# Kernel optimization log

Hardware: AMD Instinct MI355X
Metric: run time of the kernel (lower is better)

## Reference

```python
import jax, jax.numpy as jnp
import numpy as np

B, S, D, H, O = 2048, 512, 128, 64, 8
EPS = 1e-5


def setup_inputs() -> dict:
    key = jax.random.key(0)
    ks = jax.random.split(key, 8)
    sc = lambda k, shape, s: jax.random.normal(k, shape, jnp.float32) * s
    return {
        "x": jax.random.normal(ks[0], (B, S, D), jnp.float32),
        "h0": jnp.zeros((1, B, H), jnp.float32),
        # nn.RNN params (single layer, relu nonlinearity)
        "W_ih": sc(ks[1], (H, D), 1.0 / np.sqrt(H)),
        "W_hh": sc(ks[2], (H, H), 1.0 / np.sqrt(H)),
        "b_ih": jnp.zeros((H,), jnp.float32),
        "b_hh": jnp.zeros((H,), jnp.float32),
        # fc head: BatchNorm1d(H) -> Linear(H, H//4) -> ReLU
        "bn1_g": jnp.ones((H,), jnp.float32),
        "bn1_b": jnp.zeros((H,), jnp.float32),
        "fc1_W": sc(ks[3], (H // 4, H), 1.0 / np.sqrt(H)),
        "fc1_b": jnp.zeros((H // 4,), jnp.float32),
        # fc2 head: BatchNorm1d(H//4) -> Linear(H//4, O)
        "bn2_g": jnp.ones((H // 4,), jnp.float32),
        "bn2_b": jnp.zeros((H // 4,), jnp.float32),
        "fc2_W": sc(ks[4], (O, H // 4), 1.0 / np.sqrt(H // 4)),
        "fc2_b": jnp.zeros((O,), jnp.float32),
    }


def _batchnorm(x, g, b):
    # BatchNorm1d in training mode: batch statistics over the batch dim.
    mu = x.mean(0)
    var = x.var(0)  # biased variance, matching torch normalization
    return (x - mu) * jax.lax.rsqrt(var + EPS) * g + b


def reference(x, h0, W_ih, W_hh, b_ih, b_hh, bn1_g, bn1_b, fc1_W, fc1_b,
              bn2_g, bn2_b, fc2_W, fc2_b):
    # Precompute the input projection for all timesteps in one big GEMM.
    xp = jnp.einsum('bsd,hd->sbh', x, W_ih) + b_ih + b_hh  # [S, B, H]

    def step(h, xt):
        h = jax.nn.relu(xt + h @ W_hh.T)  # [B, H]
        return h, None

    hT, _ = jax.lax.scan(step, h0[0], xp)  # last hidden == out[:, -1, :]

    z = _batchnorm(hT, bn1_g, bn1_b)
    z = jax.nn.relu(z @ fc1_W.T + fc1_b)
    z = _batchnorm(z, bn2_g, bn2_b)
    out = z @ fc2_W.T + fc2_b  # [B, O]
    return out, hT[None]  # hidden_state shaped [num_layers, B, H]
```

## Files before the change

### kernel.cpp

```cpp
#include <hip/hip_runtime.h>

#define B_ 2048
#define S_ 512
#define D_ 128
#define H_ 64
#define O_ 8
#define EPS 1e-5f

#define CHUNK 16
#define NCHUNK (S_ / CHUNK)
#define PSTRIDE 68

typedef __attribute__((ext_vector_type(8))) short bf16x8;
typedef __attribute__((ext_vector_type(4))) float f32x4;

__device__ __forceinline__ unsigned pk_bf16(float a, float b) {
  unsigned ua = __builtin_bit_cast(unsigned, a) + 0x8000u;
  unsigned ub = __builtin_bit_cast(unsigned, b) + 0x8000u;
  return (ua >> 16) | (ub & 0xffff0000u);
}

__device__ __forceinline__ bf16x8 pack8(f32x4 a, f32x4 b) {
  union { bf16x8 v; unsigned u[4]; } t;
  t.u[0] = pk_bf16(a[0], a[1]);
  t.u[1] = pk_bf16(a[2], a[3]);
  t.u[2] = pk_bf16(b[0], b[1]);
  t.u[3] = pk_bf16(b[2], b[3]);
  return t.v;
}

__global__ __launch_bounds__(512, 2) void rnn_fused(
    const float* __restrict__ x, const float* __restrict__ h0,
    const float* __restrict__ W_ih, const float* __restrict__ W_hh,
    const float* __restrict__ b_ih, const float* __restrict__ b_hh,
    float* __restrict__ hT) {
  extern __shared__ float Plds[];
  const int tid = threadIdx.x;
  const int w = tid >> 6;
  const int lane = tid & 63;
  const int q = lane >> 4;
  const int c = lane & 15;
  const int row = blockIdx.x * 16 + c;

  const float* xrow = x + (size_t)row * (S_ * D_) + q * 8;
  bf16x8 Aih[4][4];
  f32x4 bias[4];
  bf16x8 Ahh[4][2];
  bf16x8 Bh[2];
  f32x4 acc[4];

  if (w < 7) {
#pragma unroll
    for (int jt = 0; jt < 4; ++jt)
#pragma unroll
      for (int kt = 0; kt < 4; ++kt) {
        const float* p = W_ih + (jt * 16 + c) * D_ + kt * 32 + q * 8;
        Aih[jt][kt] = pack8(*(const f32x4*)p, *(const f32x4*)(p + 4));
      }
#pragma unroll
    for (int jt = 0; jt < 4; ++jt) {
      f32x4 bi = *(const f32x4*)(b_ih + jt * 16 + q * 4);
      f32x4 bh = *(const f32x4*)(b_hh + jt * 16 + q * 4);
      bias[jt] = bi + bh;
    }
  } else {
#pragma unroll
    for (int jt = 0; jt < 4; ++jt)
#pragma unroll
      for (int kt = 0; kt < 2; ++kt) {
        const float* p = W_hh + (jt * 16 + c) * H_ + kt * 32 + q * 4;
        Ahh[jt][kt] = pack8(*(const f32x4*)p, *(const f32x4*)(p + 16));
      }
    const float* h0r = h0 + (size_t)row * H_;
#pragma unroll
    for (int kt = 0; kt < 2; ++kt)
      Bh[kt] = pack8(*(const f32x4*)(h0r + kt * 32 + q * 4),
                     *(const f32x4*)(h0r + kt * 32 + 16 + q * 4));
  }

  f32x4 xb[2][8];
  auto loadx = [&](f32x4* d, int t) {
    const float* p = xrow + (size_t)t * D_;
#pragma unroll
    for (int kt = 0; kt < 4; ++kt) {
      d[2 * kt]     = *(const f32x4*)(p + kt * 32);
      d[2 * kt + 1] = *(const f32x4*)(p + kt * 32 + 4);
    }
  };

  auto pstep = [&](const f32x4* xd, int s, int buf) {
    bf16x8 Bx[4];
#pragma unroll
    for (int kt = 0; kt < 4; ++kt) Bx[kt] = pack8(xd[2 * kt], xd[2 * kt + 1]);
    f32x4 a[4];
#pragma unroll
    for (int jt = 0; jt < 4; ++jt) a[jt] = bias[jt];
#pragma unroll
    for (int kt = 0; kt < 4; ++kt)
#pragma unroll
      for (int jt = 0; jt < 4; ++jt)
        a[jt] = __builtin_amdgcn_mfma_f32_16x16x32_bf16(Aih[jt][kt], Bx[kt], a[jt], 0, 0, 0);
    float* dst = Plds + ((size_t)(buf * CHUNK + s) * 16 + c) * PSTRIDE + q * 4;
#pragma unroll
    for (int jt = 0; jt < 4; ++jt)
      *(f32x4*)(dst + jt * 16) = a[jt];
  };

  const int ns = (CHUNK - 1 - w) / 7 + 1;
  auto produce = [&](int ck, int buf) {
    const int t0 = ck * CHUNK;
    loadx(xb[0], t0 + w);
#pragma unroll
    for (int i = 0; i < 3; ++i) {
      if (i < ns) {
        if (i + 1 < ns) loadx(xb[(i + 1) & 1], t0 + w + 7 * (i + 1));
        pstep(xb[i & 1], w + 7 * i, buf);
      }
    }
  };

  auto consume = [&](int buf) {
    const float* Pb = Plds + (size_t)buf * CHUNK * 16 * PSTRIDE + c * PSTRIDE + q * 4;
    f32x4 accP[4];
#pragma unroll
    for (int jt = 0; jt < 4; ++jt) accP[jt] = *(const f32x4*)(Pb + jt * 16);
#pragma unroll 1
    for (int s = 0; s < CHUNK; ++s) {
      f32x4 accN[4];
#pragma unroll
      for (int jt = 0; jt < 4; ++jt) accN[jt] = accP[jt];
      if (s + 1 < CHUNK) {
        const float* Pn = Pb + (size_t)(s + 1) * 16 * PSTRIDE;
#pragma unroll
        for (int jt = 0; jt < 4; ++jt) accN[jt] = *(const f32x4*)(Pn + jt * 16);
      }
#pragma unroll
      for (int jt = 0; jt < 4; ++jt)
        acc[jt] = __builtin_amdgcn_mfma_f32_16x16x32_bf16(Ahh[jt][0], Bh[0], accP[jt], 0, 0, 0);
#pragma unroll
      for (int jt = 0; jt < 4; ++jt)
        acc[jt] = __builtin_amdgcn_mfma_f32_16x16x32_bf16(Ahh[jt][1], Bh[1], acc[jt], 0, 0, 0);
#pragma unroll
      for (int jt = 0; jt < 4; ++jt)
#pragma unroll
        for (int e = 0; e < 4; ++e)
          acc[jt][e] = __builtin_fmaxf(acc[jt][e], 0.0f);
      Bh[0] = pack8(acc[0], acc[1]);
      Bh[1] = pack8(acc[2], acc[3]);
#pragma unroll
      for (int jt = 0; jt < 4; ++jt) accP[jt] = accN[jt];
    }
  };

  if (w < 7) produce(0, 0);
  __syncthreads();
  for (int ck = 0; ck < NCHUNK; ++ck) {
    if (w < 7) {
      if (ck + 1 < NCHUNK) produce(ck + 1, (ck + 1) & 1);
    } else {
      consume(ck & 1);
    }
    __syncthreads();
  }

  if (w == 7) {
    float* op = hT + (size_t)row * H_;
#pragma unroll
    for (int jt = 0; jt < 4; ++jt)
      *(f32x4*)(op + jt * 16 + q * 4) = acc[jt];
  }
}

__global__ void bn1_stats(const float* __restrict__ hT, float* __restrict__ ws) {
  __shared__ float ls[4][64], ls2[4][64];
  int tid = threadIdx.x;
  int j = tid & 63, rg = tid >> 6;
  int b0 = blockIdx.x * 128;
  float s = 0.f, s2 = 0.f;
  for (int i = 0; i < 32; ++i) {
    float v = hT[(size_t)(b0 + rg + i * 4) * H_ + j];
    s += v; s2 += v * v;
  }
  ls[rg][j] = s; ls2[rg][j] = s2;
  __syncthreads();
  if (tid < 64) {
    float a = ls[0][tid] + ls[1][tid] + ls[2][tid] + ls[3][tid];
    float a2 = ls2[0][tid] + ls2[1][tid] + ls2[2][tid] + ls2[3][tid];
    atomicAdd(&ws[tid], a);
    atomicAdd(&ws[64 + tid], a2);
  }
}

__global__ void fc1_bn2(const float* __restrict__ hT, const float* __restrict__ bn1_g,
                        const float* __restrict__ bn1_b, const float* __restrict__ fc1_W,
                        const float* __restrict__ fc1_b, float* __restrict__ ws) {
  __shared__ float sh[1024], sw[1024], sc[64], sf[64], zz[256];
  int tid = threadIdx.x;
  int base = blockIdx.x * 1024;
  for (int i = tid; i < 1024; i += 256) { sh[i] = hT[base + i]; sw[i] = fc1_W[i]; }
  if (tid < 64) {
    float m = ws[tid] * (1.f / B_);
    float v = ws[64 + tid] * (1.f / B_) - m * m;
    float scl = bn1_g[tid] * rsqrtf(v + EPS);
    sc[tid] = scl;
    sf[tid] = bn1_b[tid] - m * scl;
  }
  __syncthreads();
  int r = tid >> 4, f = tid & 15;
  float a = fc1_b[f];
#pragma unroll 16
  for (int j = 0; j < 64; ++j)
    a += (sh[r * 64 + j] * sc[j] + sf[j]) * sw[f * 64 + j];
  a = fmaxf(a, 0.f);
  ws[160 + blockIdx.x * 256 + tid] = a;
  zz[tid] = a;
  __syncthreads();
  if (tid < 16) {
    float s = 0.f, s2 = 0.f;
    for (int rr = 0; rr < 16; ++rr) { float v = zz[rr * 16 + tid]; s += v; s2 += v * v; }
    atomicAdd(&ws[128 + tid], s);
    atomicAdd(&ws[144 + tid], s2);
  }
}

__global__ void fc2_out(const float* __restrict__ ws, const float* __restrict__ bn2_g,
                        const float* __restrict__ bn2_b, const float* __restrict__ fc2_W,
                        const float* __restrict__ fc2_b, float* __restrict__ out) {
  __shared__ float sc2[16], sf2[16], w2[128], b2[8];
  int tid = threadIdx.x;
  if (tid < 16) {
    float m = ws[128 + tid] * (1.f / B_);
    float v = ws[144 + tid] * (1.f / B_) - m * m;
    float scl = bn2_g[tid] * rsqrtf(v + EPS);
    sc2[tid] = scl;
    sf2[tid] = bn2_b[tid] - m * scl;
  }
  if (tid < 128) w2[tid] = fc2_W[tid];
  if (tid < 8) b2[tid] = fc2_b[tid];
  __syncthreads();
  int gid = blockIdx.x * 256 + tid;
  int r = gid >> 3, o = gid & 7;
  const float* z = ws + 160 + r * 16;
  float a = b2[o];
#pragma unroll
  for (int f = 0; f < 16; ++f)
    a += (z[f] * sc2[f] + sf2[f]) * w2[o * 16 + f];
  out[gid] = a;
}

extern "C" void kernel_launch(void* const* d_in, const int* in_sizes, int n_in,
                              void* d_out, int out_size, void* d_ws, size_t ws_size,
                              hipStream_t stream) {
  (void)in_sizes; (void)n_in; (void)out_size; (void)ws_size;
  const float* x     = (const float*)d_in[0];
  const float* h0    = (const float*)d_in[1];
  const float* W_ih  = (const float*)d_in[2];
  const float* W_hh  = (const float*)d_in[3];
  const float* b_ih  = (const float*)d_in[4];
  const float* b_hh  = (const float*)d_in[5];
  const float* bn1_g = (const float*)d_in[6];
  const float* bn1_b = (const float*)d_in[7];
  const float* fc1_W = (const float*)d_in[8];
  const float* fc1_b = (const float*)d_in[9];
  const float* bn2_g = (const float*)d_in[10];
  const float* bn2_b = (const float*)d_in[11];
  const float* fc2_W = (const float*)d_in[12];
  const float* fc2_b = (const float*)d_in[13];

  float* out = (float*)d_out;
  float* hT  = out + B_ * O_;
  float* ws  = (float*)d_ws;

  const int pbytes = 2 * CHUNK * 16 * PSTRIDE * 4;
  static bool attr_done = false;
  hipFuncSetAttribute((const void*)rnn_fused,
                      hipFuncAttributeMaxDynamicSharedMemorySize, pbytes);
  (void)attr_done;

  hipMemsetAsync(d_ws, 0, 160 * sizeof(float), stream);
  rnn_fused<<<B_ / 16, 512, pbytes, stream>>>(x, h0, W_ih, W_hh, b_ih, b_hh, hT);
  bn1_stats<<<16, 256, 0, stream>>>(hT, ws);
  fc1_bn2<<<128, 256, 0, stream>>>(hT, bn1_g, bn1_b, fc1_W, fc1_b, ws);
  fc2_out<<<64, 256, 0, stream>>>(ws, bn2_g, bn2_b, fc2_W, fc2_b, out);
}
```

Before: 746.0 us.

## Halve batch rows per block to double grid size and fuse BN1 stats

Each block of the recurrent kernel now handles 8 batch rows instead of 16, so the grid grows from 128 to 256 blocks and fills more compute units, while half of each MFMA tile's columns hold padding. Invalid lanes skip their x loads and LDS stores and work on zeros or duplicated h0 rows. The separate BN1 statistics kernel is removed: the consumer wave reduces sums and sums of squares with shuffles and adds them atomically, which saves one launch and a reread of hT. The cost is wasted MFMA throughput and more global atomics.

Result: no change. 751.8 us (+0.8%).

```diff
diff --git a/kernel.cpp b/kernel.cpp
--- a/kernel.cpp
+++ b/kernel.cpp
@@ -9,6 +9,7 @@
 
 #define CHUNK 16
 #define NCHUNK (S_ / CHUNK)
+#define ROWS 8
 #define PSTRIDE 68
 
 typedef __attribute__((ext_vector_type(8))) short bf16x8;
@@ -33,14 +34,16 @@
     const float* __restrict__ x, const float* __restrict__ h0,
     const float* __restrict__ W_ih, const float* __restrict__ W_hh,
     const float* __restrict__ b_ih, const float* __restrict__ b_hh,
-    float* __restrict__ hT) {
+    float* __restrict__ hT, float* __restrict__ ws) {
   extern __shared__ float Plds[];
   const int tid = threadIdx.x;
   const int w = tid >> 6;
   const int lane = tid & 63;
   const int q = lane >> 4;
   const int c = lane & 15;
-  const int row = blockIdx.x * 16 + c;
+  const bool rv = (c < ROWS);
+  const int row = blockIdx.x * ROWS + c;
+  const int rowc = blockIdx.x * ROWS + (c & (ROWS - 1));
 
   const float* xrow = x + (size_t)row * (S_ * D_) + q * 8;
   bf16x8 Aih[4][4];
@@ -71,7 +74,7 @@
         const float* p = W_hh + (jt * 16 + c) * H_ + kt * 32 + q * 4;
         Ahh[jt][kt] = pack8(*(const f32x4*)p, *(const f32x4*)(p + 16));
       }
-    const float* h0r = h0 + (size_t)row * H_;
+    const float* h0r = h0 + (size_t)rowc * H_;
 #pragma unroll
     for (int kt = 0; kt < 2; ++kt)
       Bh[kt] = pack8(*(const f32x4*)(h0r + kt * 32 + q * 4),
@@ -79,7 +82,13 @@
   }
 
   f32x4 xb[2][8];
+#pragma unroll
+  for (int i = 0; i < 2; ++i)
+#pragma unroll
+    for (int j = 0; j < 8; ++j) xb[i][j] = (f32x4){0.f, 0.f, 0.f, 0.f};
+
   auto loadx = [&](f32x4* d, int t) {
+    if (!rv) return;
     const float* p = xrow + (size_t)t * D_;
 #pragma unroll
     for (int kt = 0; kt < 4; ++kt) {
@@ -100,10 +109,12 @@
 #pragma unroll
       for (int jt = 0; jt < 4; ++jt)
         a[jt] = __builtin_amdgcn_mfma_f32_16x16x32_bf16(Aih[jt][kt], Bx[kt], a[jt], 0, 0, 0);
-    float* dst = Plds + ((size_t)(buf * CHUNK + s) * 16 + c) * PSTRIDE + q * 4;
-#pragma unroll
-    for (int jt = 0; jt < 4; ++jt)
-      *(f32x4*)(dst + jt * 16) = a[jt];
+    if (rv) {
+      float* dst = Plds + ((size_t)(buf * CHUNK + s) * ROWS + c) * PSTRIDE + q * 4;
+#pragma unroll
+      for (int jt = 0; jt < 4; ++jt)
+        *(f32x4*)(dst + jt * 16) = a[jt];
+    }
   };
 
   const int ns = (CHUNK - 1 - w) / 7 + 1;
@@ -120,7 +131,7 @@
   };
 
   auto consume = [&](int buf) {
-    const float* Pb = Plds + (size_t)buf * CHUNK * 16 * PSTRIDE + c * PSTRIDE + q * 4;
+    const float* Pb = Plds + ((size_t)buf * CHUNK * ROWS + (c & (ROWS - 1))) * PSTRIDE + q * 4;
     f32x4 accP[4];
 #pragma unroll
     for (int jt = 0; jt < 4; ++jt) accP[jt] = *(const f32x4*)(Pb + jt * 16);
@@ -130,7 +141,7 @@
 #pragma unroll
       for (int jt = 0; jt < 4; ++jt) accN[jt] = accP[jt];
       if (s + 1 < CHUNK) {
-        const float* Pn = Pb + (size_t)(s + 1) * 16 * PSTRIDE;
+        const float* Pn = Pb + (size_t)(s + 1) * ROWS * PSTRIDE;
 #pragma unroll
         for (int jt = 0; jt < 4; ++jt) accN[jt] = *(const f32x4*)(Pn + jt * 16);
       }
@@ -164,30 +175,28 @@
   }
 
   if (w == 7) {
-    float* op = hT + (size_t)row * H_;
+    if (rv) {
+      float* op = hT + (size_t)row * H_;
+#pragma unroll
+      for (int jt = 0; jt < 4; ++jt)
+        *(f32x4*)(op + jt * 16 + q * 4) = acc[jt];
+    }
 #pragma unroll
     for (int jt = 0; jt < 4; ++jt)
-      *(f32x4*)(op + jt * 16 + q * 4) = acc[jt];
-  }
-}
-
-__global__ void bn1_stats(const float* __restrict__ hT, float* __restrict__ ws) {
-  __shared__ float ls[4][64], ls2[4][64];
-  int tid = threadIdx.x;
-  int j = tid & 63, rg = tid >> 6;
-  int b0 = blockIdx.x * 128;
-  float s = 0.f, s2 = 0.f;
-  for (int i = 0; i < 32; ++i) {
-    float v = hT[(size_t)(b0 + rg + i * 4) * H_ + j];
-    s += v; s2 += v * v;
-  }
-  ls[rg][j] = s; ls2[rg][j] = s2;
-  __syncthreads();
-  if (tid < 64) {
-    float a = ls[0][tid] + ls[1][tid] + ls[2][tid] + ls[3][tid];
-    float a2 = ls2[0][tid] + ls2[1][tid] + ls2[2][tid] + ls2[3][tid];
-    atomicAdd(&ws[tid], a);
-    atomicAdd(&ws[64 + tid], a2);
+#pragma unroll
+      for (int e = 0; e < 4; ++e) {
+        float v = rv ? acc[jt][e] : 0.f;
+        float vv = v * v;
+#pragma unroll
+        for (int m = 1; m < 8; m <<= 1) {
+          v  += __shfl_xor(v,  m, 64);
+          vv += __shfl_xor(vv, m, 64);
+        }
+        if (c == 0) {
+          atomicAdd(&ws[jt * 16 + q * 4 + e], v);
+          atomicAdd(&ws[64 + jt * 16 + q * 4 + e], vv);
+        }
+      }
   }
 }
 
@@ -271,15 +280,12 @@
   float* hT  = out + B_ * O_;
   float* ws  = (float*)d_ws;
 
-  const int pbytes = 2 * CHUNK * 16 * PSTRIDE * 4;
-  static bool attr_done = false;
+  const int pbytes = 2 * CHUNK * ROWS * PSTRIDE * 4;
   hipFuncSetAttribute((const void*)rnn_fused,
                       hipFuncAttributeMaxDynamicSharedMemorySize, pbytes);
-  (void)attr_done;
 
   hipMemsetAsync(d_ws, 0, 160 * sizeof(float), stream);
-  rnn_fused<<<B_ / 16, 512, pbytes, stream>>>(x, h0, W_ih, W_hh, b_ih, b_hh, hT);
-  bn1_stats<<<16, 256, 0, stream>>>(hT, ws);
+  rnn_fused<<<B_ / ROWS, 512, pbytes, stream>>>(x, h0, W_ih, W_hh, b_ih, b_hh, hT, ws);
   fc1_bn2<<<128, 256, 0, stream>>>(hT, bn1_g, bn1_b, fc1_W, fc1_b, ws);
   fc2_out<<<64, 256, 0, stream>>>(ws, bn2_g, bn2_b, fc2_W, fc2_b, out);
 }
```
